# Performance work log

Measured on AMD Instinct MI355X. Metric: run time of the kernel, lower is better.

The kernel has to match this reference:

```python
import jax, jax.numpy as jnp
import numpy as np

N = 200000      # total points
B = 4           # number of point clouds
C_IN = 128
C_OUT = 256
GRID = 0.05
EPS = 1e-5      # BatchNorm eps


def setup_inputs() -> dict:
    key = jax.random.key(0)
    ks = jax.random.split(key, 9)
    xyz = jax.random.uniform(ks[0], (1, N, 3), dtype=jnp.float32)
    features = jax.random.normal(ks[1], (1, N, C_IN), dtype=jnp.float32)
    offset = jnp.array([50000, 100000, 150000, 200000], dtype=jnp.int32)
    W1 = jax.random.normal(ks[2], (C_OUT, C_IN), dtype=jnp.float32) * 0.02
    b1 = jax.random.normal(ks[3], (C_OUT,), dtype=jnp.float32) * 0.01
    gamma = jax.random.uniform(ks[4], (C_OUT,), dtype=jnp.float32, minval=0.5, maxval=1.5)
    beta = jax.random.normal(ks[5], (C_OUT,), dtype=jnp.float32) * 0.1
    W2 = jax.random.normal(ks[6], (C_OUT, C_OUT), dtype=jnp.float32) * 0.02
    b2 = jax.random.normal(ks[7], (C_OUT,), dtype=jnp.float32) * 0.01
    return {"xyz": xyz, "features": features, "offset": offset,
            "W1": W1, "b1": b1, "gamma": gamma, "beta": beta, "W2": W2, "b2": b2}


def _offset2batch(offset, n):
    counts = jnp.diff(jnp.concatenate([jnp.zeros((1,), offset.dtype), offset]))
    return jnp.repeat(jnp.arange(offset.shape[0], dtype=jnp.int32), counts,
                      total_repeat_length=n)


def reference(xyz, features, offset, W1, b1, gamma, beta, W2, b2):
    pos = xyz[0]          # [N, 3]
    x = features[0]       # [N, C_IN]
    batch = _offset2batch(offset, pos.shape[0])  # [N]

    # fc: 1x1 conv == linear; BatchNorm1d in training mode (batch stats, biased var)
    h = x @ W1.T + b1                                   # [N, C_OUT]
    mu = h.mean(axis=0)
    var = h.var(axis=0)
    h = (h - mu) / jnp.sqrt(var + EPS) * gamma + beta
    h = jax.nn.relu(h)
    feats = h @ W2.T + b2                               # [N, C_OUT]

    # per-batch min corner (start)
    start = jax.ops.segment_min(pos, batch, num_segments=B)   # [B, 3]

    # voxel grid clustering
    coords = jnp.floor((pos - start[batch]) / GRID).astype(jnp.int32)  # [N, 3] >= 0
    dims = coords.max(axis=0) + 1
    lin = ((batch * dims[0] + coords[:, 0]) * dims[1] + coords[:, 1]) * dims[2] + coords[:, 2]

    uniq, inv, counts = jnp.unique(lin, return_inverse=True, return_counts=True)
    M = uniq.shape[0]

    # segment_csr mean / max over voxels (order-independent, equals sorted CSR reduce)
    xyz_out = jax.ops.segment_sum(pos, inv, num_segments=M) / counts[:, None].astype(pos.dtype)
    feat_out = jax.ops.segment_max(feats, inv, num_segments=M)

    seg_batch = jax.ops.segment_max(batch, inv, num_segments=M)
    offset_out = jnp.cumsum(jnp.bincount(seg_batch, length=B)).astype(offset.dtype)

    return (xyz_out[None], feat_out[None], offset_out, inv)
```

## Files before the change

kernel.cpp:

```cpp
#include <hip/hip_runtime.h>
#include <stdint.h>

#define GRID_SZ 0.05f
#define BN_EPS 1e-5f
#define FLAG_MAGIC 0x7FECA110

typedef __attribute__((ext_vector_type(8))) short bf16x8;
typedef __attribute__((ext_vector_type(4))) float f32x4;

#define WS_START   0
#define WS_DIMS    96
#define WS_CHSUM   128
#define WS_CHSQ    1152
#define WS_AC      2176
#define WS_BC      3200
#define WS_W1B     4224
#define WS_W2B     69760
#define WS_GRAM    200832
#define WS_CSUM    266368
#define WS_HIST    266880
#define WS_RANK    529024
#define WS_CURS    791296
#define WS_BSUM    1053440
#define WS_XYZS    1053952
#define WS_LIN     1840384
#define WS_PERM    2640384
#define WS_XB      3440384

__device__ __forceinline__ short f2bf(float f) {
  unsigned u = __float_as_uint(f);
  u += 0x7FFFu + ((u >> 16) & 1u);
  return (short)(u >> 16);
}

__device__ __forceinline__ bf16x8 load_frag(const float* p) {
  f32x4 a = *(const f32x4*)p;
  f32x4 b = *(const f32x4*)(p + 4);
  bf16x8 r;
  r[0] = f2bf(a[0]); r[1] = f2bf(a[1]); r[2] = f2bf(a[2]); r[3] = f2bf(a[3]);
  r[4] = f2bf(b[0]); r[5] = f2bf(b[1]); r[6] = f2bf(b[2]); r[7] = f2bf(b[3]);
  return r;
}

__device__ __forceinline__ int batch_of(int p, const int* offs, int nb) {
  int b = 0;
  while (b < nb - 1 && p >= offs[b]) b++;
  return b;
}

__device__ __forceinline__ float dec16(unsigned e) {
  unsigned us = (e & 0x8000u) ? (e & 0x7FFFu) : (~e & 0xFFFFu);
  return __uint_as_float(us << 16);
}

__device__ __forceinline__ void dims_of(const unsigned* gstart, int nb,
                                        int& m0, int& m1, int& m2) {
  m0 = 0; m1 = 0; m2 = 0;
  for (int b = 0; b < nb; b++) {
    float s0 = __uint_as_float(gstart[b * 3 + 0]);
    float s1 = __uint_as_float(gstart[b * 3 + 1]);
    float s2 = __uint_as_float(gstart[b * 3 + 2]);
    float x0 = __uint_as_float(gstart[12 + b * 3 + 0]);
    float x1 = __uint_as_float(gstart[12 + b * 3 + 1]);
    float x2 = __uint_as_float(gstart[12 + b * 3 + 2]);
    m0 = max(m0, (int)floorf((x0 - s0) / GRID_SZ));
    m1 = max(m1, (int)floorf((x1 - s1) / GRID_SZ));
    m2 = max(m2, (int)floorf((x2 - s2) / GRID_SZ));
  }
}

__global__ void k_init(unsigned* featU, size_t featN, int* hist, float* xyzs,
                       float* chsum, float* chsq, float* gram, float* csum,
                       unsigned* gstart,
                       const float* __restrict__ W1, const float* __restrict__ W2,
                       short* __restrict__ W1b, short* __restrict__ W2b) {
  size_t i = (size_t)blockIdx.x * blockDim.x + threadIdx.x;
  size_t stride = (size_t)gridDim.x * blockDim.x;
  if (i < 4096) *(bf16x8*)(W1b + i * 8) = load_frag(W1 + i * 8);
  else if (i < 12288) { size_t j = i - 4096; *(bf16x8*)(W2b + j * 8) = load_frag(W2 + j * 8); }
  for (size_t j = i; j < featN; j += stride) featU[j] = 0u;
  for (size_t j = i; j < 65536; j += stride) hist[j] = 0;
  for (size_t j = i; j < 65536u * 3; j += stride) xyzs[j] = 0.f;
  for (size_t j = i; j < 16384; j += stride) gram[j] = 0.f;
  if (i < 256) { chsum[i] = 0.f; chsq[i] = 0.f; }
  if (i < 128) csum[i] = 0.f;
  if (i < 12) gstart[i] = 0x7F800000u;
  else if (i < 24) gstart[i] = 0u;
}

__global__ void k_min(const float* __restrict__ pos, const int* __restrict__ offs,
                      int N, int nb, unsigned* gstart) {
  __shared__ unsigned smin[12], smax[12];
  int tid = threadIdx.x;
  if (tid < 12) { smin[tid] = 0x7F800000u; smax[tid] = 0u; }
  __syncthreads();
  int p = blockIdx.x * blockDim.x + tid;
  if (p < N) {
    int b = batch_of(p, offs, nb);
    for (int c = 0; c < 3; c++) {
      unsigned u = __float_as_uint(pos[p * 3 + c]);
      atomicMin(&smin[b * 3 + c], u);
      atomicMax(&smax[b * 3 + c], u);
    }
  }
  __syncthreads();
  if (tid < 3 * nb) {
    atomicMin(&gstart[tid], smin[tid]);
    atomicMax(&gstart[12 + tid], smax[tid]);
  }
}

__global__ void k_hist(const float* __restrict__ pos, const int* __restrict__ offs,
                       int N, int nb, const unsigned* gstart,
                       int* lin, int* hist, float* xyzs, int* gdims) {
  int m0, m1, m2;
  dims_of(gstart, nb, m0, m1, m2);
  int p = blockIdx.x * blockDim.x + threadIdx.x;
  if (blockIdx.x == 0 && threadIdx.x == 0) { gdims[0] = m0; gdims[1] = m1; gdims[2] = m2; }
  if (p >= N) return;
  int b = batch_of(p, offs, nb);
  int d0 = m0 + 1, d1 = m1 + 1, d2 = m2 + 1;
  int c[3];
  for (int i = 0; i < 3; i++) {
    float s = __uint_as_float(gstart[b * 3 + i]);
    c[i] = (int)floorf((pos[p * 3 + i] - s) / GRID_SZ);
  }
  int li = ((b * d0 + c[0]) * d1 + c[1]) * d2 + c[2];
  if (li < 0 || li >= 65536) li = 0;
  lin[p] = li;
  atomicAdd(&hist[li], 1);
  atomicAdd(&xyzs[li * 3 + 0], pos[p * 3 + 0]);
  atomicAdd(&xyzs[li * 3 + 1], pos[p * 3 + 1]);
  atomicAdd(&xyzs[li * 3 + 2], pos[p * 3 + 2]);
}

__global__ __launch_bounds__(1024) void k_scanA(const int* __restrict__ hist,
                                                const int* __restrict__ gdims, int nb,
                                                int2* bsum) {
  __shared__ int so[16], sc2[16];
  int d0 = gdims[0] + 1, d1 = gdims[1] + 1, d2 = gdims[2] + 1;
  int bins = nb * d0 * d1 * d2;
  if (bins > 65536) bins = 65536;
  int i = blockIdx.x * 1024 + threadIdx.x;
  int o = 0, c = 0;
  if (i < bins) { int h = hist[i]; o = (h > 0); c = h; }
  for (int d = 1; d < 64; d <<= 1) { o += __shfl_xor(o, d); c += __shfl_xor(c, d); }
  int w = threadIdx.x >> 6;
  if ((threadIdx.x & 63) == 0) { so[w] = o; sc2[w] = c; }
  __syncthreads();
  if (threadIdx.x == 0) {
    int O = 0, C = 0;
    for (int k = 0; k < 16; k++) { O += so[k]; C += sc2[k]; }
    bsum[blockIdx.x] = make_int2(O, C);
  }
}

__global__ __launch_bounds__(1024) void k_scanB(const int* __restrict__ hist,
                                                const int* __restrict__ gdims, int nb,
                                                const int2* __restrict__ bsum,
                                                int* rank, int* cursor,
                                                const float* __restrict__ xyzs,
                                                float* __restrict__ out_xyz,
                                                float* __restrict__ out_off) {
  __shared__ int so[1024], sc2[1024];
  __shared__ int sbase[2];
  int d0 = gdims[0] + 1, d1 = gdims[1] + 1, d2 = gdims[2] + 1;
  int bins = nb * d0 * d1 * d2;
  if (bins > 65536) bins = 65536;
  int b = blockIdx.x;
  int tid = threadIdx.x;
  if (tid == 0) {
    int O = 0, C = 0;
    for (int k = 0; k < b; k++) { int2 s = bsum[k]; O += s.x; C += s.y; }
    sbase[0] = O; sbase[1] = C;
  }
  int i = b * 1024 + tid;
  int h = (i < bins) ? hist[i] : 0;
  int o = (h > 0), c = h;
  so[tid] = o; sc2[tid] = c;
  __syncthreads();
  for (int off = 1; off < 1024; off <<= 1) {
    int vo = (tid >= off) ? so[tid - off] : 0;
    int vc = (tid >= off) ? sc2[tid - off] : 0;
    __syncthreads();
    so[tid] += vo; sc2[tid] += vc;
    __syncthreads();
  }
  if (i < bins) {
    int rk = sbase[0] + so[tid] - o;
    rank[i]   = rk;
    cursor[i] = sbase[1] + sc2[tid] - c;
    if (h > 0) {
      float fc = (float)h;
      out_xyz[rk * 3 + 0] = xyzs[i * 3 + 0] / fc;
      out_xyz[rk * 3 + 1] = xyzs[i * 3 + 1] / fc;
      out_xyz[rk * 3 + 2] = xyzs[i * 3 + 2] / fc;
    }
    int dxyz = d0 * d1 * d2;
    for (int t = 0; t < nb; t++) {
      int idx = (t + 1) * dxyz; if (idx > bins) idx = bins;
      if (idx < bins) { if (i == idx) out_off[t] = (float)rk; }
      else if (i == bins - 1) out_off[t] = (float)(sbase[0] + so[tid]);
    }
  }
  if (i == bins - 1) rank[bins] = sbase[0] + so[tid];
}

template <bool XBF>
__global__ void k_scatter(const int* __restrict__ lin, const int* __restrict__ rank,
                          int* cursor, int N, const float* __restrict__ X,
                          short* __restrict__ Xb, int* __restrict__ permvox,
                          float* __restrict__ out_inv) {
  int p = blockIdx.x * blockDim.x + threadIdx.x;
  if (p >= N) return;
  int li = lin[p];
  int r = rank[li];
  out_inv[p] = (float)r;
  int slot = atomicAdd(&cursor[li], 1);
  if (XBF) {
    permvox[slot] = r;
    const float* src = X + (size_t)p * 128;
    short* dst = Xb + (size_t)slot * 128;
#pragma unroll
    for (int j = 0; j < 16; j++)
      *(bf16x8*)(dst + j * 8) = load_frag(src + j * 8);
  } else {
    permvox[slot] = p;
  }
}

__global__ void k_initb(const int* __restrict__ permvox, int N,
                        unsigned* __restrict__ featU) {
  int inst = blockIdx.x;
  int k = inst >> 1;
  int s = k * 64 + ((inst & 1) ? 63 : 0);
  if (s >= N) s = N - 1;
  int v = permvox[s];
  featU[(size_t)v * 256 + threadIdx.x] = 0u;
}

#define GCHUNK 1024
#define XTSZ (128 * 72)
__global__ __launch_bounds__(256, 2) void k_gram(const short* __restrict__ Xb, int N,
                                                 float* __restrict__ gram,
                                                 float* __restrict__ csum) {
  __shared__ short xt[2 * XTSZ];
  __shared__ float lcs[128];
  int tid = threadIdx.x;
  int wid = tid >> 6, lane = tid & 63;
  int lr = lane & 15, lg = lane >> 4;
  int base = blockIdx.x * GCHUNK;
  int cg = tid & 7;
  int r0 = tid >> 3;
  int r1 = (tid + 256) >> 3;
  int rsA = r0 ^ (cg << 3), rsB = r1 ^ (cg << 3);
  float cs[16];
#pragma unroll
  for (int j = 0; j < 16; j++) cs[j] = 0.f;
  f32x4 acc[2][8];
#pragma unroll
  for (int a = 0; a < 2; a++)
#pragma unroll
    for (int b = 0; b < 8; b++) acc[a][b] = (f32x4){0.f, 0.f, 0.f, 0.f};

  {
    bf16x8 a0 = {0,0,0,0,0,0,0,0}, a1 = a0, b0 = a0, b1 = a0;
    int rowA = base + r0, rowB = base + r1;
    if (rowA < N) {
      const short* s = Xb + (size_t)rowA * 128 + cg * 16;
      a0 = *(const bf16x8*)s; a1 = *(const bf16x8*)(s + 8);
    }
    if (rowB < N) {
      const short* s = Xb + (size_t)rowB * 128 + cg * 16;
      b0 = *(const bf16x8*)s; b1 = *(const bf16x8*)(s + 8);
    }
#pragma unroll
    for (int j = 0; j < 8; j++) {
      cs[j]     += __uint_as_float(((unsigned)(unsigned short)a0[j]) << 16)
                 + __uint_as_float(((unsigned)(unsigned short)b0[j]) << 16);
      cs[j + 8] += __uint_as_float(((unsigned)(unsigned short)a1[j]) << 16)
                 + __uint_as_float(((unsigned)(unsigned short)b1[j]) << 16);
    }
#pragma unroll
    for (int j = 0; j < 8; j++) {
      xt[(cg * 16 + j) * 72 + rsA]     = a0[j];
      xt[(cg * 16 + 8 + j) * 72 + rsA] = a1[j];
      xt[(cg * 16 + j) * 72 + rsB]     = b0[j];
      xt[(cg * 16 + 8 + j) * 72 + rsB] = b1[j];
    }
  }

  int nst = GCHUNK / 64;
  for (int st = 0; st < nst; st++) {
    short* cur = xt + (st & 1) * XTSZ;
    short* nxt = xt + ((st & 1) ^ 1) * XTSZ;
    __syncthreads();
    bf16x8 a0 = {0,0,0,0,0,0,0,0}, a1 = a0, b0 = a0, b1 = a0;
    bool hn = (st + 1 < nst);
    if (hn) {
      int rowA = base + (st + 1) * 64 + r0;
      int rowB = base + (st + 1) * 64 + r1;
      if (rowA < N) {
        const short* s = Xb + (size_t)rowA * 128 + cg * 16;
        a0 = *(const bf16x8*)s; a1 = *(const bf16x8*)(s + 8);
      }
      if (rowB < N) {
        const short* s = Xb + (size_t)rowB * 128 + cg * 16;
        b0 = *(const bf16x8*)s; b1 = *(const bf16x8*)(s + 8);
      }
    }
#pragma unroll
    for (int ks = 0; ks < 2; ks++) {
      int kk = ks * 32 + lg * 8;
      bf16x8 f[8], af[2];
#pragma unroll
      for (int s = 0; s < 8; s++)
        f[s] = *(const bf16x8*)(cur + (s * 16 + lr) * 72 + (kk ^ (s << 3)));
#pragma unroll
      for (int a = 0; a < 2; a++) {
        int ti = wid * 2 + a;
        af[a] = *(const bf16x8*)(cur + (ti * 16 + lr) * 72 + (kk ^ (ti << 3)));
      }
#pragma unroll
      for (int a = 0; a < 2; a++)
#pragma unroll
        for (int b = 0; b < 8; b++)
          acc[a][b] = __builtin_amdgcn_mfma_f32_16x16x32_bf16(af[a], f[b], acc[a][b], 0, 0, 0);
    }
    if (hn) {
#pragma unroll
      for (int j = 0; j < 8; j++) {
        cs[j]     += __uint_as_float(((unsigned)(unsigned short)a0[j]) << 16)
                   + __uint_as_float(((unsigned)(unsigned short)b0[j]) << 16);
        cs[j + 8] += __uint_as_float(((unsigned)(unsigned short)a1[j]) << 16)
                   + __uint_as_float(((unsigned)(unsigned short)b1[j]) << 16);
      }
#pragma unroll
      for (int j = 0; j < 8; j++) {
        nxt[(cg * 16 + j) * 72 + rsA]     = a0[j];
        nxt[(cg * 16 + 8 + j) * 72 + rsA] = a1[j];
        nxt[(cg * 16 + j) * 72 + rsB]     = b0[j];
        nxt[(cg * 16 + 8 + j) * 72 + rsB] = b1[j];
      }
    }
  }
#pragma unroll
  for (int a = 0; a < 2; a++)
#pragma unroll
    for (int b = 0; b < 8; b++)
#pragma unroll
      for (int r_ = 0; r_ < 4; r_++) {
        int ci = (wid * 2 + a) * 16 + lg * 4 + r_;
        int cj = b * 16 + lr;
        atomicAdd(&gram[ci * 128 + cj], acc[a][b][r_]);
      }
  if (tid < 128) lcs[tid] = 0.f;
  __syncthreads();
#pragma unroll
  for (int j = 0; j < 16; j++) atomicAdd(&lcs[cg * 16 + j], cs[j]);
  __syncthreads();
  if (tid < 128) atomicAdd(&csum[tid], lcs[tid]);
}

__global__ __launch_bounds__(128) void k_finalizeG(const float* __restrict__ gram,
                                                   const float* __restrict__ csum,
                                                   const float* __restrict__ W1,
                                                   const float* __restrict__ b1,
                                                   const float* __restrict__ gamma,
                                                   const float* __restrict__ beta,
                                                   int N, float* Ac, float* Bc) {
  __shared__ float w[128], red[128], red2[128];
  int c = blockIdx.x, j = threadIdx.x;
  w[j] = W1[c * 128 + j];
  __syncthreads();
  float t = 0.f;
  for (int k = 0; k < 128; k++) t += gram[k * 128 + j] * w[k];
  red[j]  = t * w[j];
  red2[j] = w[j] * csum[j];
  __syncthreads();
  for (int off = 64; off > 0; off >>= 1) {
    if (j < off) { red[j] += red[j + off]; red2[j] += red2[j + off]; }
    __syncthreads();
  }
  if (j == 0) {
    float fn = (float)N;
    float q  = red[0] / fn;
    float md = red2[0] / fn;
    float b  = b1[c];
    float mu = md + b;
    float e2 = q + 2.f * b * md + b * b;
    float var = e2 - mu * mu;
    float s = gamma[c] * rsqrtf(var + BN_EPS);
    Ac[c] = s;
    Bc[c] = (b - mu) * s + beta[c];
  }
}

__global__ __launch_bounds__(256) void k_statsA(const float* __restrict__ X,
                                                const short* __restrict__ W1b,
                                                const float* __restrict__ b1, int N,
                                                float* chsum, float* chsq) {
  int tid = threadIdx.x;
  int wid = tid >> 6, lane = tid & 63;
  int lr = lane & 15, lg = lane >> 4;
  int p0 = blockIdx.x * 64;
  int wcol = wid * 64;
  f32x4 acc[4][4] = {};
  for (int kk = 0; kk < 4; kk++) {
    int k = kk * 32 + lg * 8;
    bf16x8 af[4], bfr[4];
    for (int m = 0; m < 4; m++) {
      int row = p0 + m * 16 + lr; if (row >= N) row = N - 1;
      af[m] = load_frag(X + (size_t)row * 128 + k);
    }
    for (int n = 0; n < 4; n++)
      bfr[n] = *(const bf16x8*)(W1b + (size_t)(wcol + n * 16 + lr) * 128 + k);
    for (int m = 0; m < 4; m++)
      for (int n = 0; n < 4; n++)
        acc[m][n] = __builtin_amdgcn_mfma_f32_16x16x32_bf16(af[m], bfr[n], acc[m][n], 0, 0, 0);
  }
  for (int n = 0; n < 4; n++) {
    int c = wcol + n * 16 + lr;
    float bv = b1[c];
    float s1 = 0.f, s2 = 0.f;
    for (int m = 0; m < 4; m++)
      for (int r = 0; r < 4; r++) {
        int row = p0 + m * 16 + lg * 4 + r;
        if (row < N) {
          float h = acc[m][n][r] + bv;
          s1 += h; s2 += h * h;
        }
      }
    s1 += __shfl_xor(s1, 16); s2 += __shfl_xor(s2, 16);
    s1 += __shfl_xor(s1, 32); s2 += __shfl_xor(s2, 32);
    if (lg == 0) { atomicAdd(&chsum[c], s1); atomicAdd(&chsq[c], s2); }
  }
}

__global__ void k_finalize(const float* chsum, const float* chsq, const float* b1,
                           const float* gamma, const float* beta, int N,
                           float* Ac, float* Bc) {
  int c = threadIdx.x;
  float fn = (float)N;
  float mu = chsum[c] / fn;
  float var = chsq[c] / fn - mu * mu;
  float s = gamma[c] * rsqrtf(var + BN_EPS);
  Ac[c] = s;
  Bc[c] = (b1[c] - mu) * s + beta[c];
}

template <bool XBF>
__global__ __launch_bounds__(256, 3) void k_gemmB(const float* __restrict__ X,
                                                  const short* __restrict__ Xb,
                                                  const short* __restrict__ W1b,
                                                  const short* __restrict__ W2b,
                                                  const float* __restrict__ b2,
                                                  const float* __restrict__ Ac,
                                                  const float* __restrict__ Bc,
                                                  const int* __restrict__ permvox,
                                                  const int* __restrict__ lin,
                                                  const int* __restrict__ rank,
                                                  int N, unsigned* __restrict__ featU,
                                                  int* __restrict__ bflag) {
  __shared__ char smem[64 * 264 * 2];
  __shared__ int vox_s[64];
  __shared__ int perm_s[64];
  char* axt  = smem;
  char* ylds = smem;
  unsigned short* lmax = (unsigned short*)smem;

  int tid = threadIdx.x;
  int wid = tid >> 6, lane = tid & 63;
  int lr = lane & 15, lg = lane >> 4;
  int p0 = blockIdx.x * 64;
  int wcol = wid * 64;

  if (tid < 64) {
    int s = p0 + tid;
    if (XBF) {
      vox_s[tid] = (s < N) ? permvox[s] : -1;
    } else {
      int pp = permvox[(s < N) ? s : (N - 1)];
      perm_s[tid] = pp;
      vox_s[tid] = (s < N) ? rank[lin[pp]] : -1;
    }
  }
  __syncthreads();

  {
    int row = tid >> 2, chunk = tid & 3;
    int base = row * 256 + chunk * 64;
    int sw = (row & 7) << 4;
    bf16x8 a0, a1, a2, a3;
    if (XBF) {
      int grow = p0 + row; if (grow >= N) grow = N - 1;
      const short* src = Xb + (size_t)grow * 128 + chunk * 32;
      a0 = *(const bf16x8*)(src);
      a1 = *(const bf16x8*)(src + 8);
      a2 = *(const bf16x8*)(src + 16);
      a3 = *(const bf16x8*)(src + 24);
    } else {
      int prow = perm_s[row];
      const float* src = X + (size_t)prow * 128 + chunk * 32;
      a0 = load_frag(src);
      a1 = load_frag(src + 8);
      a2 = load_frag(src + 16);
      a3 = load_frag(src + 24);
    }
    *(bf16x8*)(axt + ((base)      ^ sw)) = a0;
    *(bf16x8*)(axt + ((base + 16) ^ sw)) = a1;
    *(bf16x8*)(axt + ((base + 32) ^ sw)) = a2;
    *(bf16x8*)(axt + ((base + 48) ^ sw)) = a3;
  }
  __syncthreads();

  f32x4 acc[4][4] = {};
  for (int kk = 0; kk < 4; kk++) {
    int kbyte = kk * 64 + lg * 16;
    bf16x8 af[4], bfr[4];
    int sw = (lr & 7) << 4;
    for (int m = 0; m < 4; m++) {
      int rowA = m * 16 + lr;
      af[m] = *(const bf16x8*)(axt + ((rowA * 256 + kbyte) ^ sw));
    }
    int k = kk * 32 + lg * 8;
    for (int n = 0; n < 4; n++)
      bfr[n] = *(const bf16x8*)(W1b + (size_t)(wcol + n * 16 + lr) * 128 + k);
    for (int m = 0; m < 4; m++)
      for (int n = 0; n < 4; n++)
        acc[m][n] = __builtin_amdgcn_mfma_f32_16x16x32_bf16(af[m], bfr[n], acc[m][n], 0, 0, 0);
  }
  __syncthreads();

  for (int n = 0; n < 4; n++) {
    int c = wcol + n * 16 + lr;
    float Av = Ac[c], Bv = Bc[c];
    int colb = c * 2;
    for (int m = 0; m < 4; m++)
      for (int r = 0; r < 4; r++) {
        int row = m * 16 + lg * 4 + r;
        float y = fmaxf(acc[m][n][r] * Av + Bv, 0.0f);
        int addr = (row * 512 + colb) ^ ((row & 7) << 4);
        *(short*)(ylds + addr) = f2bf(y);
      }
  }
  __syncthreads();

  f32x4 acc2[4][4] = {};
  for (int kk = 0; kk < 8; kk++) {
    int k = kk * 32 + lg * 8;
    int kb = k * 2;
    bf16x8 af[4], bfr[4];
    for (int m = 0; m < 4; m++) {
      int row = m * 16 + lr;
      af[m] = *(const bf16x8*)(ylds + ((row * 512 + kb) ^ ((row & 7) << 4)));
    }
    for (int n = 0; n < 4; n++)
      bfr[n] = *(const bf16x8*)(W2b + (size_t)(wcol + n * 16 + lr) * 256 + k);
    for (int m = 0; m < 4; m++)
      for (int n = 0; n < 4; n++)
        acc2[m][n] = __builtin_amdgcn_mfma_f32_16x16x32_bf16(af[m], bfr[n], acc2[m][n], 0, 0, 0);
  }
  __syncthreads();

  for (int n = 0; n < 4; n++) {
    int c = wcol + n * 16 + lr;
    float bv = b2[c];
    for (int m = 0; m < 4; m++)
      for (int r = 0; r < 4; r++) {
        int row = m * 16 + lg * 4 + r;
        unsigned us = (unsigned)(unsigned short)f2bf(acc2[m][n][r] + bv);
        us = (us & 0x8000u) ? (~us & 0xFFFFu) : (us | 0x8000u);
        lmax[row * 264 + c] = (unsigned short)us;
      }
  }
  __syncthreads();

  int nrows = N - p0; if (nrows > 64) nrows = 64;
  int c = tid;
  unsigned run = 0;
  int vprev = vox_s[0];
  int run_start = 0;
  for (int row = 0; row < nrows; row++) {
    int v = vox_s[row];
    if (v != vprev) {
      size_t idx = (size_t)vprev * 256 + c;
      if (run_start > 0) {
        ((float*)featU)[idx] = dec16(run);
      } else {
        atomicMax(&featU[idx], run << 16);
        if (tid == 0) bflag[vprev] = FLAG_MAGIC;
      }
      run = 0; vprev = v; run_start = row;
    }
    run = max(run, (unsigned)lmax[row * 264 + c]);
  }
  if (vprev >= 0) {
    atomicMax(&featU[(size_t)vprev * 256 + c], run << 16);
    if (tid == 0) bflag[vprev] = FLAG_MAGIC;
  }
}

__global__ void k_decode(unsigned* featU, const int* __restrict__ bflag, size_t n) {
  size_t i = (size_t)blockIdx.x * blockDim.x + threadIdx.x;
  size_t stride = (size_t)gridDim.x * blockDim.x;
  for (; i < n; i += stride) {
    if (bflag[i >> 8] == FLAG_MAGIC) {
      unsigned e = featU[i] >> 16;
      ((float*)featU)[i] = dec16(e);
    }
  }
}

extern "C" void kernel_launch(void* const* d_in, const int* in_sizes, int n_in,
                              void* d_out, int out_size, void* d_ws, size_t ws_size,
                              hipStream_t stream) {
  const float* xyz   = (const float*)d_in[0];
  const float* X     = (const float*)d_in[1];
  const int*   offs  = (const int*)d_in[2];
  const float* W1    = (const float*)d_in[3];
  const float* b1    = (const float*)d_in[4];
  const float* gamma = (const float*)d_in[5];
  const float* beta  = (const float*)d_in[6];
  const float* W2    = (const float*)d_in[7];
  const float* b2    = (const float*)d_in[8];

  int N  = in_sizes[0] / 3;
  int nb = in_sizes[2];
  int M  = (out_size - nb - N) / 259;
  if (M <= 0) return;

  char* ws = (char*)d_ws;
  unsigned* gstart = (unsigned*)(ws + WS_START);
  int*   gdims  = (int*)(ws + WS_DIMS);
  float* chsum  = (float*)(ws + WS_CHSUM);
  float* chsq   = (float*)(ws + WS_CHSQ);
  float* Ac     = (float*)(ws + WS_AC);
  float* Bc     = (float*)(ws + WS_BC);
  short* W1b    = (short*)(ws + WS_W1B);
  short* W2b    = (short*)(ws + WS_W2B);
  float* gram   = (float*)(ws + WS_GRAM);
  float* csum   = (float*)(ws + WS_CSUM);
  int*   hist   = (int*)(ws + WS_HIST);
  int*   rank   = (int*)(ws + WS_RANK);
  int*   cursor = (int*)(ws + WS_CURS);
  int2*  bsum   = (int2*)(ws + WS_BSUM);
  float* xyzs   = (float*)(ws + WS_XYZS);
  int*   lin    = (int*)(ws + WS_LIN);
  int*   permvox = (int*)(ws + WS_PERM);
  short* Xb     = (short*)(ws + WS_XB);

  size_t req = (size_t)WS_XB + (size_t)N * 128 * 2;
  bool xbf = ws_size >= req;

  float* out_xyz  = (float*)d_out;
  float* out_feat = out_xyz + (size_t)3 * M;
  float* out_off  = out_feat + (size_t)M * 256;
  float* out_inv  = out_off + nb;
  unsigned* featU = (unsigned*)out_feat;

  int npb = (N + 255) / 256;
  int ngb = (N + 63) / 64;
  int ngr = (N + GCHUNK - 1) / GCHUNK;

  hipLaunchKernelGGL(k_init, dim3(2048), dim3(256), 0, stream,
                     featU, xbf ? (size_t)0 : (size_t)M * 256, hist, xyzs,
                     chsum, chsq, gram, csum, gstart, W1, W2, W1b, W2b);
  hipLaunchKernelGGL(k_min, dim3(npb), dim3(256), 0, stream, xyz, offs, N, nb, gstart);
  hipLaunchKernelGGL(k_hist, dim3(npb), dim3(256), 0, stream,
                     xyz, offs, N, nb, gstart, lin, hist, xyzs, gdims);
  hipLaunchKernelGGL(k_scanA, dim3(64), dim3(1024), 0, stream, hist, gdims, nb, bsum);
  hipLaunchKernelGGL(k_scanB, dim3(64), dim3(1024), 0, stream,
                     hist, gdims, nb, bsum, rank, cursor, xyzs, out_xyz, out_off);
  if (xbf) {
    hipLaunchKernelGGL((k_scatter<true>), dim3(npb), dim3(256), 0, stream,
                       lin, rank, cursor, N, X, Xb, permvox, out_inv);
    hipLaunchKernelGGL(k_initb, dim3(2 * ngb), dim3(256), 0, stream,
                       permvox, N, featU);
    hipLaunchKernelGGL(k_gram, dim3(ngr), dim3(256), 0, stream, Xb, N, gram, csum);
    hipLaunchKernelGGL(k_finalizeG, dim3(256), dim3(128), 0, stream,
                       gram, csum, W1, b1, gamma, beta, N, Ac, Bc);
    hipLaunchKernelGGL((k_gemmB<true>), dim3(ngb), dim3(256), 0, stream,
                       X, Xb, W1b, W2b, b2, Ac, Bc, permvox, lin, rank, N, featU, cursor);
  } else {
    hipLaunchKernelGGL((k_scatter<false>), dim3(npb), dim3(256), 0, stream,
                       lin, rank, cursor, N, X, Xb, permvox, out_inv);
    hipLaunchKernelGGL(k_statsA, dim3(ngb), dim3(256), 0, stream,
                       X, W1b, b1, N, chsum, chsq);
    hipLaunchKernelGGL(k_finalize, dim3(1), dim3(256), 0, stream,
                       chsum, chsq, b1, gamma, beta, N, Ac, Bc);
    hipLaunchKernelGGL((k_gemmB<false>), dim3(ngb), dim3(256), 0, stream,
                       X, Xb, W1b, W2b, b2, Ac, Bc, permvox, lin, rank, N, featU, cursor);
  }
  hipLaunchKernelGGL(k_decode, dim3(2048), dim3(256), 0, stream,
                     featU, cursor, (size_t)M * 256);
}
```

Baseline: 293.3 us.

## Fuse voxelization stages into one cooperative kernel with grid-wide syncs

Replaces six voxelization launches with one cooperative kernel of 1024 blocks: min/max, histogram, block sums, scan, scatter/bf16 conversion and featU init, separated by grid.sync(). This removes launch gaps and inter-kernel drain between small stages. It trades that for grid barrier costs, a fixed grid that may reduce parallelism in the scatter phase, and a bsum region shifted in the workspace. The old multi-kernel path remains as a fallback when cooperative launch is unavailable or fails.

```diff
diff --git a/kernel.cpp b/kernel.cpp
--- a/kernel.cpp
+++ b/kernel.cpp
@@ -1,5 +1,8 @@
 #include <hip/hip_runtime.h>
+#include <hip/hip_cooperative_groups.h>
 #include <stdint.h>
+
+namespace cg = cooperative_groups;
 
 #define GRID_SZ 0.05f
 #define BN_EPS 1e-5f
@@ -22,10 +25,10 @@
 #define WS_RANK    529024
 #define WS_CURS    791296
 #define WS_BSUM    1053440
-#define WS_XYZS    1053952
-#define WS_LIN     1840384
-#define WS_PERM    2640384
-#define WS_XB      3440384
+#define WS_XYZS    1055488
+#define WS_LIN     1841920
+#define WS_PERM    2641920
+#define WS_XB      3441920
 
 __device__ __forceinline__ short f2bf(float f) {
   unsigned u = __float_as_uint(f);
@@ -86,6 +89,143 @@
   if (i < 128) csum[i] = 0.f;
   if (i < 12) gstart[i] = 0x7F800000u;
   else if (i < 24) gstart[i] = 0u;
+}
+
+__global__ __launch_bounds__(256, 4) void k_voxel(
+    const float* __restrict__ pos, const int* __restrict__ offs, int N, int nb,
+    unsigned* gstart, int* gdims, int* lin, int* hist, float* xyzs,
+    int2* bsum, int* rank, int* cursor,
+    const float* __restrict__ X, short* __restrict__ Xb, int* permvox,
+    float* out_inv, float* out_xyz, float* out_off, unsigned* featU) {
+  cg::grid_group grid = cg::this_grid();
+  __shared__ unsigned smin[12], smax[12];
+  __shared__ int so[256], sc2[256];
+  __shared__ int sbase[2];
+  int tid = threadIdx.x;
+  int gsize = gridDim.x * blockDim.x;
+  int gtid = blockIdx.x * blockDim.x + tid;
+
+  if (tid < 12) { smin[tid] = 0x7F800000u; smax[tid] = 0u; }
+  __syncthreads();
+  for (int p = gtid; p < N; p += gsize) {
+    int b = batch_of(p, offs, nb);
+    for (int c = 0; c < 3; c++) {
+      unsigned u = __float_as_uint(pos[p * 3 + c]);
+      atomicMin(&smin[b * 3 + c], u);
+      atomicMax(&smax[b * 3 + c], u);
+    }
+  }
+  __syncthreads();
+  if (tid < 3 * nb) {
+    atomicMin(&gstart[tid], smin[tid]);
+    atomicMax(&gstart[12 + tid], smax[tid]);
+  }
+  grid.sync();
+
+  int m0, m1, m2;
+  dims_of(gstart, nb, m0, m1, m2);
+  if (gtid == 0) { gdims[0] = m0; gdims[1] = m1; gdims[2] = m2; }
+  int d0 = m0 + 1, d1 = m1 + 1, d2 = m2 + 1;
+  int dxyz = d0 * d1 * d2;
+  int bins = nb * dxyz; if (bins > 65536) bins = 65536;
+  for (int p = gtid; p < N; p += gsize) {
+    int b = batch_of(p, offs, nb);
+    int c0 = (int)floorf((pos[p * 3 + 0] - __uint_as_float(gstart[b * 3 + 0])) / GRID_SZ);
+    int c1 = (int)floorf((pos[p * 3 + 1] - __uint_as_float(gstart[b * 3 + 1])) / GRID_SZ);
+    int c2 = (int)floorf((pos[p * 3 + 2] - __uint_as_float(gstart[b * 3 + 2])) / GRID_SZ);
+    int li = ((b * d0 + c0) * d1 + c1) * d2 + c2;
+    if (li < 0 || li >= 65536) li = 0;
+    lin[p] = li;
+    atomicAdd(&hist[li], 1);
+    atomicAdd(&xyzs[li * 3 + 0], pos[p * 3 + 0]);
+    atomicAdd(&xyzs[li * 3 + 1], pos[p * 3 + 1]);
+    atomicAdd(&xyzs[li * 3 + 2], pos[p * 3 + 2]);
+  }
+  grid.sync();
+
+  int tiles = (bins + 255) >> 8;
+  if ((int)blockIdx.x < tiles) {
+    int i = blockIdx.x * 256 + tid;
+    int h = (i < bins) ? hist[i] : 0;
+    int o = (h > 0), cc = h;
+    for (int d = 1; d < 64; d <<= 1) { o += __shfl_xor(o, d); cc += __shfl_xor(cc, d); }
+    if ((tid & 63) == 0) { so[tid >> 6] = o; sc2[tid >> 6] = cc; }
+    __syncthreads();
+    if (tid == 0) {
+      int O = 0, C = 0;
+      for (int k = 0; k < 4; k++) { O += so[k]; C += sc2[k]; }
+      bsum[blockIdx.x] = make_int2(O, C);
+    }
+  }
+  grid.sync();
+
+  if ((int)blockIdx.x < tiles) {
+    int t = blockIdx.x;
+    int2 bv = (tid < t) ? bsum[tid] : make_int2(0, 0);
+    int bo = bv.x, bc = bv.y;
+    for (int d = 1; d < 64; d <<= 1) { bo += __shfl_xor(bo, d); bc += __shfl_xor(bc, d); }
+    if ((tid & 63) == 0) { so[tid >> 6] = bo; sc2[tid >> 6] = bc; }
+    __syncthreads();
+    if (tid == 0) {
+      int O = 0, C = 0;
+      for (int k = 0; k < 4; k++) { O += so[k]; C += sc2[k]; }
+      sbase[0] = O; sbase[1] = C;
+    }
+    __syncthreads();
+    int i = t * 256 + tid;
+    int h = (i < bins) ? hist[i] : 0;
+    int o = (h > 0), cc = h;
+    so[tid] = o; sc2[tid] = cc;
+    __syncthreads();
+    for (int off = 1; off < 256; off <<= 1) {
+      int vo = (tid >= off) ? so[tid - off] : 0;
+      int vc = (tid >= off) ? sc2[tid - off] : 0;
+      __syncthreads();
+      so[tid] += vo; sc2[tid] += vc;
+      __syncthreads();
+    }
+    if (i < bins) {
+      int rk = sbase[0] + so[tid] - o;
+      rank[i]   = rk;
+      cursor[i] = sbase[1] + sc2[tid] - cc;
+      if (h > 0) {
+        float fc = (float)h;
+        out_xyz[rk * 3 + 0] = xyzs[i * 3 + 0] / fc;
+        out_xyz[rk * 3 + 1] = xyzs[i * 3 + 1] / fc;
+        out_xyz[rk * 3 + 2] = xyzs[i * 3 + 2] / fc;
+      }
+      for (int tb = 0; tb < nb; tb++) {
+        int idx = (tb + 1) * dxyz; if (idx > bins) idx = bins;
+        if (idx < bins) { if (i == idx) out_off[tb] = (float)rk; }
+        else if (i == bins - 1) out_off[tb] = (float)(sbase[0] + so[tid]);
+      }
+      if (i == bins - 1) rank[bins] = sbase[0] + so[tid];
+    }
+  }
+  grid.sync();
+
+  for (int p = gtid; p < N; p += gsize) {
+    int li = lin[p];
+    int r = rank[li];
+    out_inv[p] = (float)r;
+    int slot = atomicAdd(&cursor[li], 1);
+    permvox[slot] = r;
+    const float* src = X + (size_t)p * 128;
+    short* dst = Xb + (size_t)slot * 128;
+#pragma unroll
+    for (int j = 0; j < 16; j++)
+      *(bf16x8*)(dst + j * 8) = load_frag(src + j * 8);
+  }
+  grid.sync();
+
+  int ngb = (N + 63) >> 6;
+  for (int inst = blockIdx.x; inst < 2 * ngb; inst += gridDim.x) {
+    int k = inst >> 1;
+    int s = k * 64 + ((inst & 1) ? 63 : 0);
+    if (s >= N) s = N - 1;
+    int v = permvox[s];
+    featU[(size_t)v * 256 + tid] = 0u;
+  }
 }
 
 __global__ void k_min(const float* __restrict__ pos, const int* __restrict__ offs,
@@ -250,10 +390,10 @@
   int wid = tid >> 6, lane = tid & 63;
   int lr = lane & 15, lg = lane >> 4;
   int base = blockIdx.x * GCHUNK;
-  int cg = tid & 7;
+  int cg2 = tid & 7;
   int r0 = tid >> 3;
   int r1 = (tid + 256) >> 3;
-  int rsA = r0 ^ (cg << 3), rsB = r1 ^ (cg << 3);
+  int rsA = r0 ^ (cg2 << 3), rsB = r1 ^ (cg2 << 3);
   float cs[16];
 #pragma unroll
   for (int j = 0; j < 16; j++) cs[j] = 0.f;
@@ -267,11 +407,11 @@
     bf16x8 a0 = {0,0,0,0,0,0,0,0}, a1 = a0, b0 = a0, b1 = a0;
     int rowA = base + r0, rowB = base + r1;
     if (rowA < N) {
-      const short* s = Xb + (size_t)rowA * 128 + cg * 16;
+      const short* s = Xb + (size_t)rowA * 128 + cg2 * 16;
       a0 = *(const bf16x8*)s; a1 = *(const bf16x8*)(s + 8);
     }
     if (rowB < N) {
-      const short* s = Xb + (size_t)rowB * 128 + cg * 16;
+      const short* s = Xb + (size_t)rowB * 128 + cg2 * 16;
       b0 = *(const bf16x8*)s; b1 = *(const bf16x8*)(s + 8);
     }
 #pragma unroll
@@ -283,10 +423,10 @@
     }
 #pragma unroll
     for (int j = 0; j < 8; j++) {
-      xt[(cg * 16 + j) * 72 + rsA]     = a0[j];
-      xt[(cg * 16 + 8 + j) * 72 + rsA] = a1[j];
-      xt[(cg * 16 + j) * 72 + rsB]     = b0[j];
-      xt[(cg * 16 + 8 + j) * 72 + rsB] = b1[j];
+      xt[(cg2 * 16 + j) * 72 + rsA]     = a0[j];
+      xt[(cg2 * 16 + 8 + j) * 72 + rsA] = a1[j];
+      xt[(cg2 * 16 + j) * 72 + rsB]     = b0[j];
+      xt[(cg2 * 16 + 8 + j) * 72 + rsB] = b1[j];
     }
   }
 
@@ -301,11 +441,11 @@
       int rowA = base + (st + 1) * 64 + r0;
       int rowB = base + (st + 1) * 64 + r1;
       if (rowA < N) {
-        const short* s = Xb + (size_t)rowA * 128 + cg * 16;
+        const short* s = Xb + (size_t)rowA * 128 + cg2 * 16;
         a0 = *(const bf16x8*)s; a1 = *(const bf16x8*)(s + 8);
       }
       if (rowB < N) {
-        const short* s = Xb + (size_t)rowB * 128 + cg * 16;
+        const short* s = Xb + (size_t)rowB * 128 + cg2 * 16;
         b0 = *(const bf16x8*)s; b1 = *(const bf16x8*)(s + 8);
       }
     }
@@ -337,10 +477,10 @@
       }
 #pragma unroll
       for (int j = 0; j < 8; j++) {
-        nxt[(cg * 16 + j) * 72 + rsA]     = a0[j];
-        nxt[(cg * 16 + 8 + j) * 72 + rsA] = a1[j];
-        nxt[(cg * 16 + j) * 72 + rsB]     = b0[j];
-        nxt[(cg * 16 + 8 + j) * 72 + rsB] = b1[j];
+        nxt[(cg2 * 16 + j) * 72 + rsA]     = a0[j];
+        nxt[(cg2 * 16 + 8 + j) * 72 + rsA] = a1[j];
+        nxt[(cg2 * 16 + j) * 72 + rsB]     = b0[j];
+        nxt[(cg2 * 16 + 8 + j) * 72 + rsB] = b1[j];
       }
     }
   }
@@ -357,7 +497,7 @@
   if (tid < 128) lcs[tid] = 0.f;
   __syncthreads();
 #pragma unroll
-  for (int j = 0; j < 16; j++) atomicAdd(&lcs[cg * 16 + j], cs[j]);
+  for (int j = 0; j < 16; j++) atomicAdd(&lcs[cg2 * 16 + j], cs[j]);
   __syncthreads();
   if (tid < 128) atomicAdd(&csum[tid], lcs[tid]);
 }
@@ -663,28 +803,51 @@
   int ngb = (N + 63) / 64;
   int ngr = (N + GCHUNK - 1) / GCHUNK;
 
+  int coop = 0, dev = 0;
+  hipGetDevice(&dev);
+  hipDeviceGetAttribute(&coop, hipDeviceAttributeCooperativeLaunch, dev);
+
   hipLaunchKernelGGL(k_init, dim3(2048), dim3(256), 0, stream,
                      featU, xbf ? (size_t)0 : (size_t)M * 256, hist, xyzs,
                      chsum, chsq, gram, csum, gstart, W1, W2, W1b, W2b);
-  hipLaunchKernelGGL(k_min, dim3(npb), dim3(256), 0, stream, xyz, offs, N, nb, gstart);
-  hipLaunchKernelGGL(k_hist, dim3(npb), dim3(256), 0, stream,
-                     xyz, offs, N, nb, gstart, lin, hist, xyzs, gdims);
-  hipLaunchKernelGGL(k_scanA, dim3(64), dim3(1024), 0, stream, hist, gdims, nb, bsum);
-  hipLaunchKernelGGL(k_scanB, dim3(64), dim3(1024), 0, stream,
-                     hist, gdims, nb, bsum, rank, cursor, xyzs, out_xyz, out_off);
+
+  bool coop_done = false;
+  if (xbf && coop) {
+    void* args[] = {(void*)&xyz, (void*)&offs, (void*)&N, (void*)&nb,
+                    (void*)&gstart, (void*)&gdims, (void*)&lin, (void*)&hist,
+                    (void*)&xyzs, (void*)&bsum, (void*)&rank, (void*)&cursor,
+                    (void*)&X, (void*)&Xb, (void*)&permvox,
+                    (void*)&out_inv, (void*)&out_xyz, (void*)&out_off, (void*)&featU};
+    hipError_t e = hipLaunchCooperativeKernel((const void*)k_voxel,
+                                              dim3(1024), dim3(256), args, 0, stream);
+    coop_done = (e == hipSuccess);
+  }
+
+  if (!coop_done) {
+    hipLaunchKernelGGL(k_min, dim3(npb), dim3(256), 0, stream, xyz, offs, N, nb, gstart);
+    hipLaunchKernelGGL(k_hist, dim3(npb), dim3(256), 0, stream,
+                       xyz, offs, N, nb, gstart, lin, hist, xyzs, gdims);
+    hipLaunchKernelGGL(k_scanA, dim3(64), dim3(1024), 0, stream, hist, gdims, nb, bsum);
+    hipLaunchKernelGGL(k_scanB, dim3(64), dim3(1024), 0, stream,
+                       hist, gdims, nb, bsum, rank, cursor, xyzs, out_xyz, out_off);
+    if (xbf) {
+      hipLaunchKernelGGL((k_scatter<true>), dim3(npb), dim3(256), 0, stream,
+                         lin, rank, cursor, N, X, Xb, permvox, out_inv);
+      hipLaunchKernelGGL(k_initb, dim3(2 * ngb), dim3(256), 0, stream,
+                         permvox, N, featU);
+    } else {
+      hipLaunchKernelGGL((k_scatter<false>), dim3(npb), dim3(256), 0, stream,
+                         lin, rank, cursor, N, X, Xb, permvox, out_inv);
+    }
+  }
+
   if (xbf) {
-    hipLaunchKernelGGL((k_scatter<true>), dim3(npb), dim3(256), 0, stream,
-                       lin, rank, cursor, N, X, Xb, permvox, out_inv);
-    hipLaunchKernelGGL(k_initb, dim3(2 * ngb), dim3(256), 0, stream,
-                       permvox, N, featU);
     hipLaunchKernelGGL(k_gram, dim3(ngr), dim3(256), 0, stream, Xb, N, gram, csum);
     hipLaunchKernelGGL(k_finalizeG, dim3(256), dim3(128), 0, stream,
                        gram, csum, W1, b1, gamma, beta, N, Ac, Bc);
     hipLaunchKernelGGL((k_gemmB<true>), dim3(ngb), dim3(256), 0, stream,
                        X, Xb, W1b, W2b, b2, Ac, Bc, permvox, lin, rank, N, featU, cursor);
   } else {
-    hipLaunchKernelGGL((k_scatter<false>), dim3(npb), dim3(256), 0, stream,
-                       lin, rank, cursor, N, X, Xb, permvox, out_inv);
     hipLaunchKernelGGL(k_statsA, dim3(ngb), dim3(256), 0, stream,
                        X, W1b, b1, N, chsum, chsq);
     hipLaunchKernelGGL(k_finalize, dim3(1), dim3(256), 0, stream,
```

After: 862.1 us. 2.94x slower.
